# Performance work log

Measured on AMD Instinct MI355X. Metric: run time of the kernel, lower is better.

Reference implementation:

```python
import jax, jax.numpy as jnp
import numpy as np

N_HEADS = 16
D_EMBED = 1024
BATCH = 1
SEQ = 4096


def setup_inputs() -> dict:
    key = jax.random.key(0)
    ks = jax.random.split(key, 5)
    d = D_EMBED
    x = jax.random.normal(ks[0], (BATCH, SEQ, d), dtype=jnp.float32)
    # torch Linear weights stored as (in, out) so y = x @ W + b
    W_in = jax.random.normal(ks[1], (d, 3 * d), dtype=jnp.float32) / np.sqrt(d)
    b_in = jax.random.normal(ks[2], (3 * d,), dtype=jnp.float32) * 0.02
    W_out = jax.random.normal(ks[3], (d, d), dtype=jnp.float32) / np.sqrt(d)
    b_out = jax.random.normal(ks[4], (d,), dtype=jnp.float32) * 0.02
    return {"x": x, "W_in": W_in, "b_in": b_in, "W_out": W_out, "b_out": b_out}


def reference(x, W_in, b_in, W_out, b_out):
    B, S, d = x.shape
    H = N_HEADS
    dh = d // H
    qkv = x @ W_in + b_in                      # [B, S, 3d]
    q, k, v = jnp.split(qkv, 3, axis=-1)       # each [B, S, d]
    # [B, S, H, dh] -> [B, H, S, dh]
    q = q.reshape(B, S, H, dh).transpose(0, 2, 1, 3)
    k = k.reshape(B, S, H, dh).transpose(0, 2, 1, 3)
    v = v.reshape(B, S, H, dh).transpose(0, 2, 1, 3)
    scores = jnp.einsum("bhqd,bhkd->bhqk", q, k) / jnp.sqrt(jnp.float32(dh))
    causal = jnp.tril(jnp.ones((S, S), dtype=bool))  # True = keep
    scores = jnp.where(causal, scores, -jnp.inf)
    attn = jax.nn.softmax(scores, axis=-1)
    out = jnp.einsum("bhqk,bhkd->bhqd", attn, v)     # [B, H, S, dh]
    out = out.transpose(0, 2, 1, 3).reshape(B, S, d)
    return out @ W_out + b_out
```

## Files before the change

### kernel.cpp

```cpp
#include <hip/hip_runtime.h>
#include <stdint.h>

#define S_LEN 4096
#define D_EMB 1024
#define NH 16
#define DHEAD 64
#define N3 3072

typedef __attribute__((ext_vector_type(8))) short short8;
typedef __attribute__((ext_vector_type(4))) short short4v;
typedef __attribute__((ext_vector_type(4))) float f32x4;

#define OFF_XB    0u
#define OFF_WINT  4194304u
#define OFF_WOUTT 7340032u
#define OFF_Q     8388608u
#define OFF_ATTN  20971520u

#define QSCALE 0.1803368801111204f
#define DEFER_THR 11.0f

__device__ __forceinline__ unsigned short f2bf(float f) {
  unsigned u = __float_as_uint(f);
  unsigned r = u + 0x7FFFu + ((u >> 16) & 1u);
  return (unsigned short)(r >> 16);
}
__device__ __forceinline__ unsigned cvtpk_bf16(float lo, float hi) {
  unsigned r;
  asm("v_cvt_pk_bf16_f32 %0, %1, %2" : "=v"(r) : "v"(lo), "v"(hi));
  return r;
}
__device__ __forceinline__ void gload16(const void* g, void* l) {
  __builtin_amdgcn_global_load_lds((const __attribute__((address_space(1))) void*)g,
                                   (__attribute__((address_space(3))) void*)l, 16, 0, 0);
}

__global__ __launch_bounds__(256) void cvt_bf16_kernel(const float* __restrict__ src,
                                                       ushort* __restrict__ dst, int n) {
  int i = (blockIdx.x * 256 + threadIdx.x) * 4;
  if (i + 3 < n) {
    float4 v = *(const float4*)(src + i);
    ushort4 o;
    o.x = f2bf(v.x); o.y = f2bf(v.y); o.z = f2bf(v.z); o.w = f2bf(v.w);
    *(ushort4*)(dst + i) = o;
  }
}

__global__ __launch_bounds__(256) void transpose_cvt_kernel(const float* __restrict__ src,
                                                            ushort* __restrict__ dst,
                                                            int R, int C) {
  __shared__ float tile[32][33];
  int tx = threadIdx.x & 31, ty = threadIdx.x >> 5;
  int c0 = blockIdx.x * 32, r0 = blockIdx.y * 32;
#pragma unroll
  for (int i = 0; i < 32; i += 8)
    tile[ty + i][tx] = src[(size_t)(r0 + ty + i) * C + c0 + tx];
  __syncthreads();
#pragma unroll
  for (int i = 0; i < 32; i += 8)
    dst[(size_t)(c0 + ty + i) * R + r0 + tx] = f2bf(tile[tx][ty + i]);
}

__global__ __launch_bounds__(512, 2) void gemm1_8phase(const ushort* __restrict__ A,
                                                       const ushort* __restrict__ Bt,
                                                       const float* __restrict__ bias,
                                                       ushort* __restrict__ o16) {
  __shared__ ushort L[65536];
  const int K = 1024;
  int tid = threadIdx.x, w = tid >> 6, lane = tid & 63;
  int wr = w >> 2, wc = w & 3;
  int l15 = lane & 15, g = lane >> 4;
  int lr = lane >> 3, lc = lane & 7;
  int swcol = (lc ^ lr) * 8;
  int rxor = (l15 & 7) << 3;
  int id = blockIdx.y * 12 + blockIdx.x;
  int id2 = (id & 7) * 24 + (id >> 3);
  int bm = (id2 / 12) * 256, bn = (id2 % 12) * 256;

  f32x4 acc[8][4];
#pragma unroll
  for (int m = 0; m < 8; ++m)
#pragma unroll
    for (int n = 0; n < 4; ++n) acc[m][n] = (f32x4){0.f, 0.f, 0.f, 0.f};

  auto stageA = [&](int t, int h) {
#pragma unroll
    for (int r2 = 0; r2 < 2; ++r2)
      gload16(A + (size_t)(bm + h * 128 + r2 * 64 + w * 8 + lr) * K + t * 64 + swcol,
              &L[((t & 1) * 2 + h) * 8192 + r2 * 4096 + w * 512]);
  };
  auto stageB = [&](int t, int h) {
#pragma unroll
    for (int r2 = 0; r2 < 2; ++r2)
      gload16(Bt + (size_t)(bn + h * 128 + r2 * 64 + w * 8 + lr) * K + t * 64 + swcol,
              &L[32768 + ((t & 1) * 2 + h) * 8192 + r2 * 4096 + w * 512]);
  };

  short8 bf[4][2], af[2][2];
  auto readB = [&](int tb) {
    int base = 32768 + (tb * 2 + (wc >> 1)) * 8192 + (wc & 1) * 4096;
#pragma unroll
    for (int n = 0; n < 4; ++n)
#pragma unroll
      for (int ks = 0; ks < 2; ++ks)
        bf[n][ks] = *(const short8*)&L[base + (n * 16 + l15) * 64 + ((ks * 32 + g * 8) ^ rxor)];
  };
  auto readA2 = [&](int tb, int m0) {
    int base = (tb * 2 + wr) * 8192;
#pragma unroll
    for (int mi = 0; mi < 2; ++mi)
#pragma unroll
      for (int ks = 0; ks < 2; ++ks)
        af[mi][ks] = *(const short8*)&L[base + ((m0 + mi) * 16 + l15) * 64 + ((ks * 32 + g * 8) ^ rxor)];
  };
  auto mfma8 = [&](int m0) {
#pragma unroll
    for (int mi = 0; mi < 2; ++mi)
#pragma unroll
      for (int n = 0; n < 4; ++n)
#pragma unroll
        for (int ks = 0; ks < 2; ++ks)
          acc[m0 + mi][n] =
              __builtin_amdgcn_mfma_f32_16x16x32_bf16(af[mi][ks], bf[n][ks], acc[m0 + mi][n], 0, 0, 0);
  };

#define BAR() __builtin_amdgcn_s_barrier()
#define LGK0() asm volatile("s_waitcnt lgkmcnt(0)" ::: "memory")
#define VM4() asm volatile("s_waitcnt vmcnt(4)" ::: "memory")
#define VM0() asm volatile("s_waitcnt vmcnt(0)" ::: "memory")

  stageA(0, 0); stageA(0, 1); stageB(0, 0); stageB(0, 1);
  stageB(1, 0); stageB(1, 1);
  VM4();
  BAR();

  for (int i = 0; i < 8; ++i) {
    int T = 2 * i;
    bool more = (T + 2 < 16);
    readB(0); readA2(0, 0); stageA(T + 1, 0);
    BAR(); LGK0();
    __builtin_amdgcn_s_setprio(1); mfma8(0); __builtin_amdgcn_s_setprio(0);
    BAR();
    readA2(0, 2); stageA(T + 1, 1);
    BAR(); LGK0();
    __builtin_amdgcn_s_setprio(1); mfma8(2); __builtin_amdgcn_s_setprio(0);
    BAR();
    readA2(0, 4); if (more) stageB(T + 2, 0);
    BAR(); LGK0();
    __builtin_amdgcn_s_setprio(1); mfma8(4); __builtin_amdgcn_s_setprio(0);
    BAR();
    readA2(0, 6); if (more) stageB(T + 2, 1);
    BAR(); LGK0();
    __builtin_amdgcn_s_setprio(1); mfma8(6); __builtin_amdgcn_s_setprio(0);
    if (more) VM4(); else VM0();
    BAR();
    readB(1); readA2(1, 0); if (more) stageA(T + 2, 0);
    BAR(); LGK0();
    __builtin_amdgcn_s_setprio(1); mfma8(0); __builtin_amdgcn_s_setprio(0);
    BAR();
    readA2(1, 2); if (more) stageA(T + 2, 1);
    BAR(); LGK0();
    __builtin_amdgcn_s_setprio(1); mfma8(2); __builtin_amdgcn_s_setprio(0);
    BAR();
    readA2(1, 4); if (more) stageB(T + 3, 0);
    BAR(); LGK0();
    __builtin_amdgcn_s_setprio(1); mfma8(4); __builtin_amdgcn_s_setprio(0);
    BAR();
    readA2(1, 6); if (more) stageB(T + 3, 1);
    BAR(); LGK0();
    __builtin_amdgcn_s_setprio(1); mfma8(6); __builtin_amdgcn_s_setprio(0);
    if (more) VM4(); else VM0();
    BAR();
  }
#undef BAR
#undef LGK0
#undef VM4
#undef VM0

#pragma unroll
  for (int m = 0; m < 8; ++m) {
    int rbase = bm + wr * 128 + m * 16 + g * 4;
#pragma unroll
    for (int n = 0; n < 4; ++n) {
      int c = bn + wc * 64 + n * 16 + l15;
      float bv = bias[c];
      int which = c >> 10, cc = c & 1023, hh = cc >> 6, dcol = cc & 63;
      if (which == 2) {
        ushort4 o;
        o.x = f2bf(acc[m][n][0] + bv);
        o.y = f2bf(acc[m][n][1] + bv);
        o.z = f2bf(acc[m][n][2] + bv);
        o.w = f2bf(acc[m][n][3] + bv);
        *(ushort4*)&o16[8388608u + (size_t)hh * (DHEAD * (size_t)S_LEN) +
                        (size_t)dcol * S_LEN + rbase] = o;
      } else {
        float qs = (which == 0) ? QSCALE : 1.0f;
        ushort* dst = o16 + (size_t)which * 4194304u +
                      (size_t)hh * (S_LEN * DHEAD) + dcol;
#pragma unroll
        for (int j = 0; j < 4; ++j)
          dst[(size_t)(rbase + j) * DHEAD] = f2bf((acc[m][n][j] + bv) * qs);
      }
    }
  }
}

#define BK 64

__global__ __launch_bounds__(256) void gemm_bt_kernel(const ushort* __restrict__ A,
                                                      const ushort* __restrict__ Bt,
                                                      const float* __restrict__ bias,
                                                      float* __restrict__ o32,
                                                      int N, int K) {
  __shared__ ushort As[128 * 64];
  __shared__ ushort Bs[128 * 64];
  int tid = threadIdx.x, w = tid >> 6, lane = tid & 63;
  int wr = w >> 1, wc = w & 1;
  int l15 = lane & 15, g = lane >> 4;
  int gx = gridDim.x;
  int id = blockIdx.y * gx + blockIdx.x;
  int q8 = (gx * gridDim.y) >> 3;
  int id2 = (id & 7) * q8 + (id >> 3);
  int bm = (id2 / gx) * 128, bn = (id2 % gx) * 128;
  f32x4 acc[4][4];
#pragma unroll
  for (int m = 0; m < 4; ++m)
#pragma unroll
    for (int n = 0; n < 4; ++n) acc[m][n] = (f32x4){0.f, 0.f, 0.f, 0.f};

  int srow = lane >> 3;
  int scol = (lane & 7) * 8;

  for (int k0 = 0; k0 < K; k0 += BK) {
    __syncthreads();
#pragma unroll
    for (int i = 0; i < 4; ++i) {
      int ch = w * 4 + i;
      int row = ch * 8 + srow;
      gload16(A + (size_t)(bm + row) * K + k0 + scol, &As[ch * 512]);
      gload16(Bt + (size_t)(bn + row) * K + k0 + scol, &Bs[ch * 512]);
    }
    __syncthreads();
    short8 a[4][2], b[4][2];
#pragma unroll
    for (int m = 0; m < 4; ++m)
#pragma unroll
      for (int t = 0; t < 2; ++t)
        a[m][t] = *(const short8*)&As[(wr * 64 + m * 16 + l15) * 64 + t * 32 + g * 8];
#pragma unroll
    for (int n = 0; n < 4; ++n)
#pragma unroll
      for (int t = 0; t < 2; ++t)
        b[n][t] = *(const short8*)&Bs[(wc * 64 + n * 16 + l15) * 64 + t * 32 + g * 8];
#pragma unroll
    for (int m = 0; m < 4; ++m)
#pragma unroll
      for (int n = 0; n < 4; ++n)
#pragma unroll
        for (int t = 0; t < 2; ++t)
          acc[m][n] = __builtin_amdgcn_mfma_f32_16x16x32_bf16(a[m][t], b[n][t], acc[m][n], 0, 0, 0);
  }

#pragma unroll
  for (int m = 0; m < 4; ++m) {
    int rbase = bm + wr * 64 + m * 16 + g * 4;
#pragma unroll
    for (int n = 0; n < 4; ++n) {
      int c = bn + wc * 64 + n * 16 + l15;
      float bv = bias[c];
#pragma unroll
      for (int j = 0; j < 4; ++j)
        o32[(size_t)(rbase + j) * N + c] = acc[m][n][j] + bv;
    }
  }
}

__global__ __launch_bounds__(512) void attn_kernel(const ushort* __restrict__ Q,
                                                   const ushort* __restrict__ Kg,
                                                   const ushort* __restrict__ Vtg,
                                                   ushort* __restrict__ O) {
  __shared__ ushort Ks[2][64 * 64];
  __shared__ ushort Vs[2][64 * 64];
  int bid = blockIdx.x;
  int h = bid & 15;
  int qt = (bid < 256) ? (31 - (bid >> 4)) : ((bid - 256) >> 4);
  int q0 = qt * 128;
  int tid = threadIdx.x, w = tid >> 6, lane = tid & 63;
  int l15 = lane & 15, g = lane >> 4;
  const ushort* qh = Q + (size_t)h * (S_LEN * DHEAD);
  const ushort* kh = Kg + (size_t)h * (S_LEN * DHEAD);
  const ushort* vh = Vtg + (size_t)h * (DHEAD * (size_t)S_LEN);
  int sr = tid >> 3;
  int scc = (tid & 7) * 8;
  int wo = sr * 64 + (((scc * 2) ^ ((sr & 7) << 4)) >> 1);
  int kxor = (l15 & 7) << 4;
  int koff0 = ((g * 16) ^ kxor) >> 1;
  int koff1 = ((64 + g * 16) ^ kxor) >> 1;
  int voff[4];
#pragma unroll
  for (int ct = 0; ct < 4; ++ct) voff[ct] = ((ct * 32 + g * 8) ^ kxor) >> 1;

  int qrow = q0 + w * 16 + l15;
  short8 aq[2];
#pragma unroll
  for (int t = 0; t < 2; ++t)
    aq[t] = *(const short8*)&qh[(size_t)qrow * DHEAD + t * 32 + g * 8];

  f32x4 acc_o[4];
#pragma unroll
  for (int dt = 0; dt < 4; ++dt) acc_o[dt] = (f32x4){0.f, 0.f, 0.f, 0.f};
  float m = -1e30f, l = 0.f;
  int last = 2 * qt + 1;

  {
    short8 ka = *(const short8*)&kh[(size_t)sr * DHEAD + scc];
    short8 va = *(const short8*)&vh[(size_t)sr * S_LEN + scc];
    *(short8*)&Ks[0][wo] = ka;
    *(short8*)&Vs[0][wo] = va;
  }
  short8 nk, nv;
  {
    nk = *(const short8*)&kh[(size_t)(64 + sr) * DHEAD + scc];
    nv = *(const short8*)&vh[(size_t)sr * S_LEN + 64 + scc];
  }
  __syncthreads();
  int cur = 0;

  for (int it = 0; it <= last; ++it) {
    int kv0 = it * 64;
    bool more = (it < last);
    const ushort* Kc = Ks[cur];
    const ushort* Vc = Vs[cur];

    f32x4 accs[4];
#pragma unroll
    for (int ct = 0; ct < 4; ++ct) accs[ct] = (f32x4){0.f, 0.f, 0.f, 0.f};
    __builtin_amdgcn_s_setprio(1);
#pragma unroll
    for (int ct = 0; ct < 4; ++ct) {
      int rb = (ct * 16 + l15) * 64;
      short8 kf0 = *(const short8*)&Kc[rb + koff0];
      short8 kf1 = *(const short8*)&Kc[rb + koff1];
      accs[ct] = __builtin_amdgcn_mfma_f32_16x16x32_bf16(kf0, aq[0], accs[ct], 0, 0, 0);
      accs[ct] = __builtin_amdgcn_mfma_f32_16x16x32_bf16(kf1, aq[1], accs[ct], 0, 0, 0);
    }
    __builtin_amdgcn_s_setprio(0);

    if (it >= 2 * qt) {
#pragma unroll
      for (int ct = 0; ct < 4; ++ct) {
        int kbase = kv0 + ct * 16 + g * 4;
#pragma unroll
        for (int j = 0; j < 4; ++j)
          if (kbase + j > qrow) accs[ct][j] = -1e30f;
      }
    }

    float a0 = fmaxf(fmaxf(accs[0][0], accs[0][1]), fmaxf(accs[0][2], accs[0][3]));
    float a1 = fmaxf(fmaxf(accs[1][0], accs[1][1]), fmaxf(accs[1][2], accs[1][3]));
    float a2 = fmaxf(fmaxf(accs[2][0], accs[2][1]), fmaxf(accs[2][2], accs[2][3]));
    float a3 = fmaxf(fmaxf(accs[3][0], accs[3][1]), fmaxf(accs[3][2], accs[3][3]));
    float pm = fmaxf(fmaxf(a0, a1), fmaxf(a2, a3));

    if (!__all(pm <= m + DEFER_THR)) {
      pm = fmaxf(pm, __shfl_xor(pm, 16));
      pm = fmaxf(pm, __shfl_xor(pm, 32));
      float mnew = fmaxf(m, pm);
      float corr = __builtin_amdgcn_exp2f(m - mnew);
      l *= corr; m = mnew;
#pragma unroll
      for (int dt = 0; dt < 4; ++dt)
#pragma unroll
        for (int j = 0; j < 4; ++j) acc_o[dt][j] *= corr;
    }

    float rs = 0.f;
    short8 pk8[2];
#pragma unroll
    for (int t2 = 0; t2 < 2; ++t2) {
      float p0 = __builtin_amdgcn_exp2f(accs[2 * t2][0] - m);
      float p1 = __builtin_amdgcn_exp2f(accs[2 * t2][1] - m);
      float p2 = __builtin_amdgcn_exp2f(accs[2 * t2][2] - m);
      float p3 = __builtin_amdgcn_exp2f(accs[2 * t2][3] - m);
      float p4 = __builtin_amdgcn_exp2f(accs[2 * t2 + 1][0] - m);
      float p5 = __builtin_amdgcn_exp2f(accs[2 * t2 + 1][1] - m);
      float p6 = __builtin_amdgcn_exp2f(accs[2 * t2 + 1][2] - m);
      float p7 = __builtin_amdgcn_exp2f(accs[2 * t2 + 1][3] - m);
      rs += ((p0 + p1) + (p2 + p3)) + ((p4 + p5) + (p6 + p7));
      union { unsigned u[4]; short8 v; } pu;
      pu.u[0] = cvtpk_bf16(p0, p1);
      pu.u[1] = cvtpk_bf16(p2, p3);
      pu.u[2] = cvtpk_bf16(p4, p5);
      pu.u[3] = cvtpk_bf16(p6, p7);
      pk8[t2] = pu.v;
    }
    l += rs;

    __builtin_amdgcn_s_setprio(1);
#pragma unroll
    for (int dt = 0; dt < 4; ++dt) {
      int rb = (dt * 16 + l15) * 64;
#pragma unroll
      for (int t2 = 0; t2 < 2; ++t2) {
        union { short4v hh[2]; short8 v; } vu;
        vu.hh[0] = *(const short4v*)&Vc[rb + voff[2 * t2]];
        vu.hh[1] = *(const short4v*)&Vc[rb + voff[2 * t2 + 1]];
        acc_o[dt] = __builtin_amdgcn_mfma_f32_16x16x32_bf16(vu.v, pk8[t2], acc_o[dt], 0, 0, 0);
      }
    }
    __builtin_amdgcn_s_setprio(0);

    if (more) {
      *(short8*)&Ks[cur ^ 1][wo] = nk;
      *(short8*)&Vs[cur ^ 1][wo] = nv;
      if (it + 2 <= last) {
        int kv2 = kv0 + 128;
        nk = *(const short8*)&kh[(size_t)(kv2 + sr) * DHEAD + scc];
        nv = *(const short8*)&vh[(size_t)sr * S_LEN + kv2 + scc];
      }
    }
    __syncthreads();
    cur ^= 1;
  }

  l += __shfl_xor(l, 16);
  l += __shfl_xor(l, 32);
  float rl = (l > 0.f) ? 1.f / l : 0.f;
#pragma unroll
  for (int dt = 0; dt < 4; ++dt) {
    ushort4 o;
    o.x = f2bf(acc_o[dt][0] * rl);
    o.y = f2bf(acc_o[dt][1] * rl);
    o.z = f2bf(acc_o[dt][2] * rl);
    o.w = f2bf(acc_o[dt][3] * rl);
    *(ushort4*)&O[(size_t)qrow * D_EMB + h * DHEAD + dt * 16 + g * 4] = o;
  }
}

extern "C" void kernel_launch(void* const* d_in, const int* in_sizes, int n_in,
                              void* d_out, int out_size, void* d_ws, size_t ws_size,
                              hipStream_t stream) {
  const float* x = (const float*)d_in[0];
  const float* W_in = (const float*)d_in[1];
  const float* b_in = (const float*)d_in[2];
  const float* W_out = (const float*)d_in[3];
  const float* b_out = (const float*)d_in[4];
  float* out = (float*)d_out;
  ushort* ws = (ushort*)d_ws;

  cvt_bf16_kernel<<<4096, 256, 0, stream>>>(x, ws + OFF_XB, S_LEN * D_EMB);
  transpose_cvt_kernel<<<dim3(N3 / 32, D_EMB / 32), 256, 0, stream>>>(W_in, ws + OFF_WINT, D_EMB, N3);
  transpose_cvt_kernel<<<dim3(D_EMB / 32, D_EMB / 32), 256, 0, stream>>>(W_out, ws + OFF_WOUTT, D_EMB, D_EMB);
  gemm1_8phase<<<dim3(12, 16), 512, 0, stream>>>(
      ws + OFF_XB, ws + OFF_WINT, b_in, ws + OFF_Q);
  attn_kernel<<<512, 512, 0, stream>>>(
      ws + OFF_Q, ws + OFF_Q + 4194304u, ws + OFF_Q + 8388608u, ws + OFF_ATTN);
  gemm_bt_kernel<<<dim3(D_EMB / 128, S_LEN / 128), 256, 0, stream>>>(
      ws + OFF_ATTN, ws + OFF_WOUTT, b_out, out, D_EMB, D_EMB);
}
```

Baseline: 139.9 us.

## Split attention KV loop across two blocks and merge partial results

The attention kernel now launches twice as many blocks. Each block processes alternating KV tiles (even or odd) and writes an unnormalized-then-normalized partial output plus its row max and sum, and a new combine kernel merges the two partials using log-sum-exp weights. This raises parallelism and shortens the critical path of long causal rows, at the cost of an extra kernel launch, extra global traffic for partials, and an extra bf16 rounding step. The output projection GEMM is also changed to 512 threads with 8 waves, each computing a 64x32 sub-tile.

```diff
diff --git a/kernel.cpp b/kernel.cpp
--- a/kernel.cpp
+++ b/kernel.cpp
@@ -24,6 +24,9 @@
   unsigned u = __float_as_uint(f);
   unsigned r = u + 0x7FFFu + ((u >> 16) & 1u);
   return (unsigned short)(r >> 16);
+}
+__device__ __forceinline__ float bf2f(unsigned short b) {
+  return __uint_as_float(((unsigned)b) << 16);
 }
 __device__ __forceinline__ unsigned cvtpk_bf16(float lo, float hi) {
   unsigned r;
@@ -207,55 +210,52 @@
 
 #define BK 64
 
-__global__ __launch_bounds__(256) void gemm_bt_kernel(const ushort* __restrict__ A,
-                                                      const ushort* __restrict__ Bt,
-                                                      const float* __restrict__ bias,
-                                                      float* __restrict__ o32,
-                                                      int N, int K) {
+__global__ __launch_bounds__(512) void gemm2_kernel(const ushort* __restrict__ A,
+                                                    const ushort* __restrict__ Bt,
+                                                    const float* __restrict__ bias,
+                                                    float* __restrict__ o32,
+                                                    int N, int K) {
   __shared__ ushort As[128 * 64];
   __shared__ ushort Bs[128 * 64];
   int tid = threadIdx.x, w = tid >> 6, lane = tid & 63;
-  int wr = w >> 1, wc = w & 1;
+  int wr = w >> 2, wc = w & 3;
   int l15 = lane & 15, g = lane >> 4;
+  int lr = lane >> 3, lc = lane & 7;
   int gx = gridDim.x;
   int id = blockIdx.y * gx + blockIdx.x;
   int q8 = (gx * gridDim.y) >> 3;
   int id2 = (id & 7) * q8 + (id >> 3);
   int bm = (id2 / gx) * 128, bn = (id2 % gx) * 128;
-  f32x4 acc[4][4];
+  f32x4 acc[4][2];
 #pragma unroll
   for (int m = 0; m < 4; ++m)
 #pragma unroll
-    for (int n = 0; n < 4; ++n) acc[m][n] = (f32x4){0.f, 0.f, 0.f, 0.f};
-
-  int srow = lane >> 3;
-  int scol = (lane & 7) * 8;
+    for (int n = 0; n < 2; ++n) acc[m][n] = (f32x4){0.f, 0.f, 0.f, 0.f};
 
   for (int k0 = 0; k0 < K; k0 += BK) {
     __syncthreads();
 #pragma unroll
-    for (int i = 0; i < 4; ++i) {
-      int ch = w * 4 + i;
-      int row = ch * 8 + srow;
-      gload16(A + (size_t)(bm + row) * K + k0 + scol, &As[ch * 512]);
-      gload16(Bt + (size_t)(bn + row) * K + k0 + scol, &Bs[ch * 512]);
+    for (int i = 0; i < 2; ++i) {
+      int row = i * 64 + w * 8 + lr;
+      gload16(A + (size_t)(bm + row) * K + k0 + lc * 8, &As[i * 4096 + w * 512]);
+      gload16(Bt + (size_t)(bn + row) * K + k0 + lc * 8, &Bs[i * 4096 + w * 512]);
     }
     __syncthreads();
-    short8 a[4][2], b[4][2];
+    short8 a[4][2], b[2][2];
 #pragma unroll
     for (int m = 0; m < 4; ++m)
 #pragma unroll
       for (int t = 0; t < 2; ++t)
         a[m][t] = *(const short8*)&As[(wr * 64 + m * 16 + l15) * 64 + t * 32 + g * 8];
 #pragma unroll
-    for (int n = 0; n < 4; ++n)
+    for (int n = 0; n < 2; ++n)
 #pragma unroll
       for (int t = 0; t < 2; ++t)
-        b[n][t] = *(const short8*)&Bs[(wc * 64 + n * 16 + l15) * 64 + t * 32 + g * 8];
+        b[n][t] = *(const short8*)&Bs[(wc * 32 + n * 16 + l15) * 64 + t * 32 + g * 8];
 #pragma unroll
     for (int m = 0; m < 4; ++m)
 #pragma unroll
-      for (int n = 0; n < 4; ++n)
+      for (int n = 0; n < 2; ++n)
 #pragma unroll
         for (int t = 0; t < 2; ++t)
           acc[m][n] = __builtin_amdgcn_mfma_f32_16x16x32_bf16(a[m][t], b[n][t], acc[m][n], 0, 0, 0);
@@ -265,8 +265,8 @@
   for (int m = 0; m < 4; ++m) {
     int rbase = bm + wr * 64 + m * 16 + g * 4;
 #pragma unroll
-    for (int n = 0; n < 4; ++n) {
-      int c = bn + wc * 64 + n * 16 + l15;
+    for (int n = 0; n < 2; ++n) {
+      int c = bn + wc * 32 + n * 16 + l15;
       float bv = bias[c];
 #pragma unroll
       for (int j = 0; j < 4; ++j)
@@ -278,18 +278,23 @@
 __global__ __launch_bounds__(512) void attn_kernel(const ushort* __restrict__ Q,
                                                    const ushort* __restrict__ Kg,
                                                    const ushort* __restrict__ Vtg,
-                                                   ushort* __restrict__ O) {
+                                                   ushort* __restrict__ P0,
+                                                   ushort* __restrict__ P1,
+                                                   float2* __restrict__ ml) {
   __shared__ ushort Ks[2][64 * 64];
   __shared__ ushort Vs[2][64 * 64];
   int bid = blockIdx.x;
-  int h = bid & 15;
-  int qt = (bid < 256) ? (31 - (bid >> 4)) : ((bid - 256) >> 4);
+  int c = bid >> 9;
+  int r = bid & 511;
+  int h = r & 15;
+  int qt = (r < 256) ? (31 - (r >> 4)) : ((r - 256) >> 4);
   int q0 = qt * 128;
   int tid = threadIdx.x, w = tid >> 6, lane = tid & 63;
   int l15 = lane & 15, g = lane >> 4;
   const ushort* qh = Q + (size_t)h * (S_LEN * DHEAD);
   const ushort* kh = Kg + (size_t)h * (S_LEN * DHEAD);
   const ushort* vh = Vtg + (size_t)h * (DHEAD * (size_t)S_LEN);
+  ushort* Pc = c ? P1 : P0;
   int sr = tid >> 3;
   int scc = (tid & 7) * 8;
   int wo = sr * 64 + (((scc * 2) ^ ((sr & 7) << 4)) >> 1);
@@ -313,22 +318,24 @@
   int last = 2 * qt + 1;
 
   {
-    short8 ka = *(const short8*)&kh[(size_t)sr * DHEAD + scc];
-    short8 va = *(const short8*)&vh[(size_t)sr * S_LEN + scc];
+    int kv0 = c * 64;
+    short8 ka = *(const short8*)&kh[(size_t)(kv0 + sr) * DHEAD + scc];
+    short8 va = *(const short8*)&vh[(size_t)sr * S_LEN + kv0 + scc];
     *(short8*)&Ks[0][wo] = ka;
     *(short8*)&Vs[0][wo] = va;
   }
   short8 nk, nv;
-  {
-    nk = *(const short8*)&kh[(size_t)(64 + sr) * DHEAD + scc];
-    nv = *(const short8*)&vh[(size_t)sr * S_LEN + 64 + scc];
+  if (c + 2 <= last) {
+    int kv2 = (c + 2) * 64;
+    nk = *(const short8*)&kh[(size_t)(kv2 + sr) * DHEAD + scc];
+    nv = *(const short8*)&vh[(size_t)sr * S_LEN + kv2 + scc];
   }
   __syncthreads();
   int cur = 0;
 
-  for (int it = 0; it <= last; ++it) {
+  for (int it = c; it <= last; it += 2) {
     int kv0 = it * 64;
-    bool more = (it < last);
+    bool more = (it + 2 <= last);
     const ushort* Kc = Ks[cur];
     const ushort* Vc = Vs[cur];
 
@@ -413,10 +420,10 @@
     if (more) {
       *(short8*)&Ks[cur ^ 1][wo] = nk;
       *(short8*)&Vs[cur ^ 1][wo] = nv;
-      if (it + 2 <= last) {
-        int kv2 = kv0 + 128;
-        nk = *(const short8*)&kh[(size_t)(kv2 + sr) * DHEAD + scc];
-        nv = *(const short8*)&vh[(size_t)sr * S_LEN + kv2 + scc];
+      if (it + 4 <= last) {
+        int kv4 = kv0 + 256;
+        nk = *(const short8*)&kh[(size_t)(kv4 + sr) * DHEAD + scc];
+        nv = *(const short8*)&vh[(size_t)sr * S_LEN + kv4 + scc];
       }
     }
     __syncthreads();
@@ -425,7 +432,8 @@
 
   l += __shfl_xor(l, 16);
   l += __shfl_xor(l, 32);
-  float rl = (l > 0.f) ? 1.f / l : 0.f;
+  bool dead = (m == -1e30f);
+  float rl = (!dead && l > 0.f) ? 1.f / l : 0.f;
 #pragma unroll
   for (int dt = 0; dt < 4; ++dt) {
     ushort4 o;
@@ -433,8 +441,37 @@
     o.y = f2bf(acc_o[dt][1] * rl);
     o.z = f2bf(acc_o[dt][2] * rl);
     o.w = f2bf(acc_o[dt][3] * rl);
-    *(ushort4*)&O[(size_t)qrow * D_EMB + h * DHEAD + dt * 16 + g * 4] = o;
-  }
+    *(ushort4*)&Pc[(size_t)qrow * D_EMB + h * DHEAD + dt * 16 + g * 4] = o;
+  }
+  if (g == 0)
+    ml[(size_t)(c * NH + h) * S_LEN + qrow] = make_float2(m, dead ? 0.f : l);
+}
+
+__global__ __launch_bounds__(256) void combine_kernel(const ushort* __restrict__ P0,
+                                                      const ushort* __restrict__ P1,
+                                                      const float2* __restrict__ ml,
+                                                      ushort* __restrict__ Out) {
+  int idx = blockIdx.x * 256 + threadIdx.x;
+  int row = idx >> 7;
+  int cb = (idx & 127) * 8;
+  int h = cb >> 6;
+  float2 e0 = ml[(size_t)h * S_LEN + row];
+  float2 e1 = ml[(size_t)(NH + h) * S_LEN + row];
+  float mm = fmaxf(e0.x, e1.x);
+  float w0 = e0.y * __builtin_amdgcn_exp2f(e0.x - mm);
+  float w1 = e1.y * __builtin_amdgcn_exp2f(e1.x - mm);
+  float inv = 1.f / (w0 + w1);
+  w0 *= inv; w1 *= inv;
+  size_t base = (size_t)row * D_EMB + cb;
+  short8 a = *(const short8*)&P0[base];
+  short8 b = *(const short8*)&P1[base];
+  short8 o;
+#pragma unroll
+  for (int i = 0; i < 8; ++i) {
+    float fv = w0 * bf2f((unsigned short)a[i]) + w1 * bf2f((unsigned short)b[i]);
+    o[i] = (short)f2bf(fv);
+  }
+  *(short8*)&Out[base] = o;
 }
 
 extern "C" void kernel_launch(void* const* d_in, const int* in_sizes, int n_in,
@@ -448,13 +485,18 @@
   float* out = (float*)d_out;
   ushort* ws = (ushort*)d_ws;
 
+  ushort* P0 = ws + OFF_ATTN;
+  ushort* P1 = ws + OFF_XB;
+  float2* ml = (float2*)(ws + OFF_WINT);
+
   cvt_bf16_kernel<<<4096, 256, 0, stream>>>(x, ws + OFF_XB, S_LEN * D_EMB);
   transpose_cvt_kernel<<<dim3(N3 / 32, D_EMB / 32), 256, 0, stream>>>(W_in, ws + OFF_WINT, D_EMB, N3);
   transpose_cvt_kernel<<<dim3(D_EMB / 32, D_EMB / 32), 256, 0, stream>>>(W_out, ws + OFF_WOUTT, D_EMB, D_EMB);
   gemm1_8phase<<<dim3(12, 16), 512, 0, stream>>>(
       ws + OFF_XB, ws + OFF_WINT, b_in, ws + OFF_Q);
-  attn_kernel<<<512, 512, 0, stream>>>(
-      ws + OFF_Q, ws + OFF_Q + 4194304u, ws + OFF_Q + 8388608u, ws + OFF_ATTN);
-  gemm_bt_kernel<<<dim3(D_EMB / 128, S_LEN / 128), 256, 0, stream>>>(
-      ws + OFF_ATTN, ws + OFF_WOUTT, b_out, out, D_EMB, D_EMB);
-}
+  attn_kernel<<<1024, 512, 0, stream>>>(
+      ws + OFF_Q, ws + OFF_Q + 4194304u, ws + OFF_Q + 8388608u, P0, P1, ml);
+  combine_kernel<<<(S_LEN * D_EMB / 8) / 256, 256, 0, stream>>>(P0, P1, ml, P0);
+  gemm2_kernel<<<dim3(D_EMB / 128, S_LEN / 128), 512, 0, stream>>>(
+      P0, ws + OFF_WOUTT, b_out, out, D_EMB, D_EMB);
+}
```

After: 148.6 us. 6.3% more time.

## Fuse input conversion kernels into one launch and halve output GEMM tile width

Applied to the files above, without the earlier changes.

The separate x-to-bf16 conversion and the two weight transpose-convert kernels are merged into one prep kernel that dispatches on block index, cutting two kernel launches and their gaps. The output projection GEMM changes from 128x128 to 128x64 tiles, doubling the grid from 256 to 512 blocks so all CUs get work on the 256-CU device. The narrower tile lowers per-block arithmetic intensity and makes A tiles get reloaded more often.

```diff
diff --git a/kernel.cpp b/kernel.cpp
--- a/kernel.cpp
+++ b/kernel.cpp
@@ -35,23 +35,36 @@
                                    (__attribute__((address_space(3))) void*)l, 16, 0, 0);
 }
 
-__global__ __launch_bounds__(256) void cvt_bf16_kernel(const float* __restrict__ src,
-                                                       ushort* __restrict__ dst, int n) {
-  int i = (blockIdx.x * 256 + threadIdx.x) * 4;
-  if (i + 3 < n) {
-    float4 v = *(const float4*)(src + i);
+__global__ __launch_bounds__(256) void prep_kernel(const float* __restrict__ x,
+                                                   const float* __restrict__ W_in,
+                                                   const float* __restrict__ W_out,
+                                                   ushort* __restrict__ xb,
+                                                   ushort* __restrict__ wint,
+                                                   ushort* __restrict__ woutt) {
+  __shared__ float tile[32][33];
+  int b = blockIdx.x;
+  if (b < 4096) {
+    int i = (b * 256 + threadIdx.x) * 4;
+    float4 v = *(const float4*)(x + i);
     ushort4 o;
     o.x = f2bf(v.x); o.y = f2bf(v.y); o.z = f2bf(v.z); o.w = f2bf(v.w);
-    *(ushort4*)(dst + i) = o;
-  }
-}
-
-__global__ __launch_bounds__(256) void transpose_cvt_kernel(const float* __restrict__ src,
-                                                            ushort* __restrict__ dst,
-                                                            int R, int C) {
-  __shared__ float tile[32][33];
+    *(ushort4*)(xb + i) = o;
+    return;
+  }
+  const float* src;
+  ushort* dst;
+  int R, C, bx, by;
+  if (b < 7168) {
+    int t = b - 4096;
+    src = W_in; dst = wint; R = D_EMB; C = N3;
+    bx = t % 96; by = t / 96;
+  } else {
+    int t = b - 7168;
+    src = W_out; dst = woutt; R = D_EMB; C = D_EMB;
+    bx = t & 31; by = t >> 5;
+  }
   int tx = threadIdx.x & 31, ty = threadIdx.x >> 5;
-  int c0 = blockIdx.x * 32, r0 = blockIdx.y * 32;
+  int c0 = bx * 32, r0 = by * 32;
 #pragma unroll
   for (int i = 0; i < 32; i += 8)
     tile[ty + i][tx] = src[(size_t)(r0 + ty + i) * C + c0 + tx];
@@ -207,13 +220,13 @@
 
 #define BK 64
 
-__global__ __launch_bounds__(256) void gemm_bt_kernel(const ushort* __restrict__ A,
-                                                      const ushort* __restrict__ Bt,
-                                                      const float* __restrict__ bias,
-                                                      float* __restrict__ o32,
-                                                      int N, int K) {
+__global__ __launch_bounds__(256) void gemm2_kernel(const ushort* __restrict__ A,
+                                                    const ushort* __restrict__ Bt,
+                                                    const float* __restrict__ bias,
+                                                    float* __restrict__ o32,
+                                                    int N, int K) {
   __shared__ ushort As[128 * 64];
-  __shared__ ushort Bs[128 * 64];
+  __shared__ ushort Bs[64 * 64];
   int tid = threadIdx.x, w = tid >> 6, lane = tid & 63;
   int wr = w >> 1, wc = w & 1;
   int l15 = lane & 15, g = lane >> 4;
@@ -221,12 +234,12 @@
   int id = blockIdx.y * gx + blockIdx.x;
   int q8 = (gx * gridDim.y) >> 3;
   int id2 = (id & 7) * q8 + (id >> 3);
-  int bm = (id2 / gx) * 128, bn = (id2 % gx) * 128;
-  f32x4 acc[4][4];
+  int bm = (id2 / gx) * 128, bn = (id2 % gx) * 64;
+  f32x4 acc[4][2];
 #pragma unroll
   for (int m = 0; m < 4; ++m)
 #pragma unroll
-    for (int n = 0; n < 4; ++n) acc[m][n] = (f32x4){0.f, 0.f, 0.f, 0.f};
+    for (int n = 0; n < 2; ++n) acc[m][n] = (f32x4){0.f, 0.f, 0.f, 0.f};
 
   int srow = lane >> 3;
   int scol = (lane & 7) * 8;
@@ -236,26 +249,29 @@
 #pragma unroll
     for (int i = 0; i < 4; ++i) {
       int ch = w * 4 + i;
-      int row = ch * 8 + srow;
-      gload16(A + (size_t)(bm + row) * K + k0 + scol, &As[ch * 512]);
-      gload16(Bt + (size_t)(bn + row) * K + k0 + scol, &Bs[ch * 512]);
+      gload16(A + (size_t)(bm + ch * 8 + srow) * K + k0 + scol, &As[ch * 512]);
+    }
+#pragma unroll
+    for (int i = 0; i < 2; ++i) {
+      int ch = w * 2 + i;
+      gload16(Bt + (size_t)(bn + ch * 8 + srow) * K + k0 + scol, &Bs[ch * 512]);
     }
     __syncthreads();
-    short8 a[4][2], b[4][2];
+    short8 a[4][2], b[2][2];
 #pragma unroll
     for (int m = 0; m < 4; ++m)
 #pragma unroll
       for (int t = 0; t < 2; ++t)
         a[m][t] = *(const short8*)&As[(wr * 64 + m * 16 + l15) * 64 + t * 32 + g * 8];
 #pragma unroll
-    for (int n = 0; n < 4; ++n)
+    for (int n = 0; n < 2; ++n)
 #pragma unroll
       for (int t = 0; t < 2; ++t)
-        b[n][t] = *(const short8*)&Bs[(wc * 64 + n * 16 + l15) * 64 + t * 32 + g * 8];
+        b[n][t] = *(const short8*)&Bs[(wc * 32 + n * 16 + l15) * 64 + t * 32 + g * 8];
 #pragma unroll
     for (int m = 0; m < 4; ++m)
 #pragma unroll
-      for (int n = 0; n < 4; ++n)
+      for (int n = 0; n < 2; ++n)
 #pragma unroll
         for (int t = 0; t < 2; ++t)
           acc[m][n] = __builtin_amdgcn_mfma_f32_16x16x32_bf16(a[m][t], b[n][t], acc[m][n], 0, 0, 0);
@@ -265,8 +281,8 @@
   for (int m = 0; m < 4; ++m) {
     int rbase = bm + wr * 64 + m * 16 + g * 4;
 #pragma unroll
-    for (int n = 0; n < 4; ++n) {
-      int c = bn + wc * 64 + n * 16 + l15;
+    for (int n = 0; n < 2; ++n) {
+      int c = bn + wc * 32 + n * 16 + l15;
       float bv = bias[c];
 #pragma unroll
       for (int j = 0; j < 4; ++j)
@@ -448,13 +464,12 @@
   float* out = (float*)d_out;
   ushort* ws = (ushort*)d_ws;
 
-  cvt_bf16_kernel<<<4096, 256, 0, stream>>>(x, ws + OFF_XB, S_LEN * D_EMB);
-  transpose_cvt_kernel<<<dim3(N3 / 32, D_EMB / 32), 256, 0, stream>>>(W_in, ws + OFF_WINT, D_EMB, N3);
-  transpose_cvt_kernel<<<dim3(D_EMB / 32, D_EMB / 32), 256, 0, stream>>>(W_out, ws + OFF_WOUTT, D_EMB, D_EMB);
+  prep_kernel<<<8192, 256, 0, stream>>>(x, W_in, W_out,
+                                        ws + OFF_XB, ws + OFF_WINT, ws + OFF_WOUTT);
   gemm1_8phase<<<dim3(12, 16), 512, 0, stream>>>(
       ws + OFF_XB, ws + OFF_WINT, b_in, ws + OFF_Q);
   attn_kernel<<<512, 512, 0, stream>>>(
       ws + OFF_Q, ws + OFF_Q + 4194304u, ws + OFF_Q + 8388608u, ws + OFF_ATTN);
-  gemm_bt_kernel<<<dim3(D_EMB / 128, S_LEN / 128), 256, 0, stream>>>(
+  gemm2_kernel<<<dim3(16, 32), 256, 0, stream>>>(
       ws + OFF_ATTN, ws + OFF_WOUTT, b_out, out, D_EMB, D_EMB);
 }
```

Result: faster. 133.8 us (-4.4%).
